# Kernel optimization log

Hardware: AMD Instinct MI355X
Metric: run time of the kernel (lower is better)

Reference implementation:

```python
import jax, jax.numpy as jnp
import numpy as np

N, n, m, k = 100000, 32, 16, 32
MU = 100.0  # bubble kernel scale (init arg mu)


def setup_inputs() -> dict:
    key = jax.random.key(0)
    ks = jax.random.split(key, 7)
    x = jax.random.normal(ks[0], (N,), dtype=jnp.float32)
    # torch.nn.Linear(N, n): weight [n, N], bias [n]
    encoder_w = jax.random.normal(ks[1], (n, N), dtype=jnp.float32) / np.float32(np.sqrt(N))
    encoder_b = jnp.zeros((n,), dtype=jnp.float32)
    # decoder parameter [n, N]
    decoder = jax.random.normal(ks[2], (n, N), dtype=jnp.float32) / np.float32(np.sqrt(n))
    # torch.nn.Linear(n, n*m): weight [n*m, n], bias [n*m]
    bw_w = jax.random.normal(ks[3], (n * m, n), dtype=jnp.float32) / np.float32(np.sqrt(n))
    bw_b = jnp.zeros((n * m,), dtype=jnp.float32)
    neighbour_distance = jax.random.uniform(ks[4], (N, k), dtype=jnp.float32)
    neighbour_id = jax.random.randint(ks[5], (N, k), 0, N)
    clustering_labels = jax.random.randint(ks[6], (N,), 0, m)
    return {
        "x": x,
        "encoder_w": encoder_w,
        "encoder_b": encoder_b,
        "decoder": decoder,
        "bw_w": bw_w,
        "bw_b": bw_b,
        "neighbour_distance": neighbour_distance,
        "neighbour_id": neighbour_id,
        "clustering_labels": clustering_labels,
    }


def reference(x, encoder_w, encoder_b, decoder, bw_w, bw_b,
              neighbour_distance, neighbour_id, clustering_labels):
    # encode: [N] -> [n]
    encoded = x @ encoder_w.T + encoder_b
    # per-basis, per-cluster bandwidths: sigmoid(Linear)/60 -> [n, m] -> expand to [n, N]
    bandwidths = jax.nn.sigmoid(encoded @ bw_w.T + bw_b) / 60.0
    w = bandwidths.reshape(n, m)[:, clustering_labels]  # [n, N]
    # bubble window: relu(1 - d^2 / (w*mu)^2) -> [n, N, k]
    window = jax.nn.relu(1.0 - neighbour_distance[None, :, :] ** 2
                         / (w[:, :, None] * MU) ** 2)
    # normalization over axis 1 (the N axis), faithful to the source's dim=1
    window = window / jnp.sum(window, axis=1, keepdims=True)
    # gather decoder rows at neighbours, weight, reduce over k: [n, N]
    convolved_basis = jnp.sum(decoder[:, neighbour_id] * window, axis=-1)
    # [n] @ [n, N] -> [N]
    return encoded @ convolved_basis
```

## Files before the change

### kernel.cpp

```cpp
#include <hip/hip_runtime.h>
#include <hip/hip_fp16.h>

#define N_PTS 100000
#define MU_F  100.0f

typedef unsigned int uint;
typedef _Float16 h2 __attribute__((ext_vector_type(2)));

#define E_SCALE 16384.0f
#define E_SCALE_INV (1.0f / 16384.0f)

#define ENC_BLKS 256
#define TR_BLKS  1563
#define HIST_BLKS 64

__global__ __launch_bounds__(256) void k_prep(const float* __restrict__ x,
                                              const float* __restrict__ encW,
                                              const float* __restrict__ encB,
                                              const float* __restrict__ dec,
                                              const int* __restrict__ labels,
                                              float* __restrict__ enc,
                                              __half* __restrict__ decT,
                                              int* __restrict__ ghist) {
    int b = blockIdx.x;
    if (b < ENC_BLKS) {
        int row = b & 31;
        int chunk = b >> 5;
        const int CH = N_PTS / 8;
        int base = chunk * CH;
        const float4* W4 = reinterpret_cast<const float4*>(encW + (size_t)row * N_PTS + base);
        const float4* x4 = reinterpret_cast<const float4*>(x + base);
        const int nv = CH / 4;
        float acc = 0.f;
        for (int idx = threadIdx.x; idx < nv; idx += 256) {
            float4 w = W4[idx];
            float4 xv = x4[idx];
            acc += w.x * xv.x + w.y * xv.y + w.z * xv.z + w.w * xv.w;
        }
        #pragma unroll
        for (int off = 32; off > 0; off >>= 1) acc += __shfl_down(acc, off);
        __shared__ float sred[4];
        int wid = threadIdx.x >> 6;
        if ((threadIdx.x & 63) == 0) sred[wid] = acc;
        __syncthreads();
        if (threadIdx.x == 0) {
            float s = sred[0] + sred[1] + sred[2] + sred[3];
            if (chunk == 0) s += encB[row];
            atomicAdd(enc + row, s);
        }
    } else if (b < ENC_BLKS + TR_BLKS) {
        __shared__ float tile[32][65];
        int j0 = (b - ENC_BLKS) * 64;
        int col = threadIdx.x & 63;
        int r0 = threadIdx.x >> 6;
        #pragma unroll
        for (int it = 0; it < 8; ++it) {
            int row = it * 4 + r0;
            int j = j0 + col;
            float v = (j < N_PTS) ? dec[(size_t)row * N_PTS + j] : 0.f;
            tile[row][col] = v;
        }
        __syncthreads();
        #pragma unroll
        for (int it = 0; it < 4; ++it) {
            int idx = it * 256 + threadIdx.x;
            int j = idx >> 4;
            int p = idx & 15;
            int jj = j0 + j;
            if (jj < N_PTS) {
                __half2 h = __halves2half2(__float2half(tile[2 * p][j]),
                                           __float2half(tile[2 * p + 1][j]));
                *reinterpret_cast<__half2*>(decT + (size_t)jj * 32 + 2 * p) = h;
            }
        }
    } else {
        __shared__ int lh[16];
        if (threadIdx.x < 16) lh[threadIdx.x] = 0;
        __syncthreads();
        int hb = b - (ENC_BLKS + TR_BLKS);
        for (int j = hb * 256 + threadIdx.x; j < N_PTS; j += HIST_BLKS * 256)
            atomicAdd(&lh[labels[j]], 1);
        __syncthreads();
        if (threadIdx.x < 16) atomicAdd(&ghist[threadIdx.x], lh[threadIdx.x]);
    }
}

__global__ __launch_bounds__(256) void k_scatter(const int* __restrict__ labels,
                                                 const int* __restrict__ ghist,
                                                 int* __restrict__ gcursor,
                                                 int* __restrict__ perm) {
    __shared__ int lh[16], lbase[16], lcur[16], gb[16];
    const int CHUNK = 784;
    int start = blockIdx.x * CHUNK;
    int end = min(start + CHUNK, N_PTS);
    if (threadIdx.x < 16) { lh[threadIdx.x] = 0; lcur[threadIdx.x] = 0; }
    if (threadIdx.x == 0) {
        int run = 0;
        for (int c = 0; c < 16; ++c) { gb[c] = run; run += ghist[c]; }
    }
    __syncthreads();
    for (int j = start + threadIdx.x; j < end; j += 256)
        atomicAdd(&lh[labels[j]], 1);
    __syncthreads();
    if (threadIdx.x < 16)
        lbase[threadIdx.x] = gb[threadIdx.x] + atomicAdd(&gcursor[threadIdx.x], lh[threadIdx.x]);
    __syncthreads();
    for (int j = start + threadIdx.x; j < end; j += 256) {
        int c = labels[j];
        int lpos = atomicAdd(&lcur[c], 1);
        perm[lbase[c] + lpos] = j;
    }
}

__device__ inline void build_invC(const float* __restrict__ encL,
                                  const float* __restrict__ bw_w,
                                  const float* __restrict__ bw_b,
                                  float* __restrict__ invCL, int c) {
    if (threadIdx.x < 32) {
        int r = threadIdx.x * 16 + c;
        float z = bw_b[r];
        const float* wr = bw_w + r * 32;
        #pragma unroll
        for (int p = 0; p < 32; ++p) z = fmaf(encL[p], wr[p], z);
        float s = 1.f / (1.f + __expf(-z));
        float wmu = s * (MU_F / 60.0f);
        invCL[threadIdx.x] = 1.f / (wmu * wmu);
    }
}

__global__ __launch_bounds__(512, 4) void k_S_sorted(const float* __restrict__ enc_g,
                                                     const float* __restrict__ bw_w,
                                                     const float* __restrict__ bw_b,
                                                     const float* __restrict__ nd,
                                                     const int* __restrict__ perm,
                                                     const int* __restrict__ ghist,
                                                     float* __restrict__ S,
                                                     float* __restrict__ S_part) {
    __shared__ float encL[32], invCL[32];
    __shared__ float Sloc[512];
    __shared__ int baseSh[17];
    int b = blockIdx.x;
    int c = b & 15;
    int ih = (b >> 4) & 1;
    int ch = b >> 5;
    if (threadIdx.x < 32) encL[threadIdx.x] = enc_g[threadIdx.x];
    if (threadIdx.x < 512) Sloc[threadIdx.x] = 0.f;
    if (threadIdx.x == 0) {
        int run = 0;
        for (int cc = 0; cc < 16; ++cc) { baseSh[cc] = run; run += ghist[cc]; }
        baseSh[16] = run;
    }
    __syncthreads();
    build_invC(encL, bw_w, bw_b, invCL, c);
    __syncthreads();

    float invC[16];
    #pragma unroll
    for (int i = 0; i < 16; ++i) invC[i] = invCL[ih * 16 + i];

    int bs = baseSh[c];
    int cnt = baseSh[c + 1] - bs;
    int lane = threadIdx.x & 63;
    int kk = lane & 31;
    int jh = lane >> 5;
    int gw = ch * 8 + (threadIdx.x >> 6);
    const int nw = 16 * 8;
    int npairs = (cnt + 1) >> 1;

    float acc[16];
    #pragma unroll
    for (int i = 0; i < 16; ++i) acc[i] = 0.f;

    for (int pp = gw; pp < npairs; pp += nw) {
        bool valid = (2 * pp + jh) < cnt;
        int p = valid ? (bs + 2 * pp + jh) : bs;
        int j = __builtin_nontemporal_load(&perm[p]);
        float d = __builtin_nontemporal_load(&nd[(size_t)j * 32 + kk]);
        float d2 = valid ? d * d : 1e30f;
        #pragma unroll
        for (int i = 0; i < 16; ++i)
            acc[i] += fmaxf(fmaf(-d2, invC[i], 1.0f), 0.f);
    }
    #pragma unroll
    for (int i = 0; i < 16; ++i) acc[i] += __shfl_xor(acc[i], 32);
    if (jh == 0) {
        #pragma unroll
        for (int i = 0; i < 16; ++i) atomicAdd(&Sloc[i * 32 + kk], acc[i]);
    }
    __syncthreads();
    if (S_part) {
        if (threadIdx.x < 512)
            S_part[(size_t)b * 512 + threadIdx.x] = Sloc[threadIdx.x];
    } else {
        if (threadIdx.x < 512) {
            float v = Sloc[threadIdx.x];
            if (v != 0.f)
                atomicAdd(&S[(ih * 16 + (threadIdx.x >> 5)) * 32 + (threadIdx.x & 31)], v);
        }
    }
}

__global__ __launch_bounds__(256) void k_S_reduce(const float* __restrict__ S_part,
                                                  float* __restrict__ S) {
    int g = blockIdx.x >> 2;
    int t = (blockIdx.x & 3) * 256 + threadIdx.x;
    int ih = t >> 9;
    int p = t & 511;
    float s = 0.f;
    #pragma unroll
    for (int c = 0; c < 16; ++c) {
        int b = c + (ih << 4) + (g << 5);
        s += S_part[(size_t)b * 512 + p];
    }
    atomicAdd(&S[t], s);
}

__global__ __launch_bounds__(256, 6) void k_main(const float* __restrict__ enc_g,
                                                 const float* __restrict__ bw_w,
                                                 const float* __restrict__ bw_b,
                                                 const float* __restrict__ S_g,
                                                 const float* __restrict__ nd,
                                                 const int* __restrict__ nid,
                                                 const int* __restrict__ perm,
                                                 const int* __restrict__ ghist,
                                                 const __half* __restrict__ decT,
                                                 float* __restrict__ out) {
    __shared__ float encL[32], invCL[32];
    __shared__ float ELf[1024];
    __shared__ int baseSh[17];
    int c = blockIdx.x & 15;
    int ch = blockIdx.x >> 4;
    if (threadIdx.x < 32) encL[threadIdx.x] = enc_g[threadIdx.x];
    if (threadIdx.x == 0) {
        int run = 0;
        for (int cc = 0; cc < 16; ++cc) { baseSh[cc] = run; run += ghist[cc]; }
        baseSh[16] = run;
    }
    __syncthreads();
    build_invC(encL, bw_w, bw_b, invCL, c);
    for (int t = threadIdx.x; t < 1024; t += 256)
        ELf[t] = encL[t >> 5] / S_g[t] * E_SCALE;
    __syncthreads();

    int lane = threadIdx.x & 63;
    int kk = lane & 31;
    int jh = lane >> 5;
    int R = lane >> 2;
    int q = lane & 3;

    float invq[8];
    h2 EhA[4], EhB[4];
    #pragma unroll
    for (int t = 0; t < 8; ++t) invq[t] = invCL[q * 8 + t];
    #pragma unroll
    for (int t = 0; t < 4; ++t) {
        int i0 = q * 8 + 2 * t, i1 = i0 + 1;
        EhA[t] = __builtin_bit_cast(h2, __builtin_amdgcn_cvt_pkrtz(
                     ELf[i0 * 32 + R], ELf[i1 * 32 + R]));
        EhB[t] = __builtin_bit_cast(h2, __builtin_amdgcn_cvt_pkrtz(
                     ELf[i0 * 32 + R + 16], ELf[i1 * 32 + R + 16]));
    }

    int bs = baseSh[c];
    int cnt = baseSh[c + 1] - bs;
    int wv = ch * 4 + (threadIdx.x >> 6);
    const int nw = 96 * 4;
    int npairs = (cnt + 1) >> 1;
    const uint4* decQ = reinterpret_cast<const uint4*>(decT);

    int pp = wv;
    int jl = 0, idl = 0; float d2l = 1e30f; bool validl = false;
    if (pp < npairs) {
        validl = (2 * pp + jh) < cnt;
        int p = validl ? (bs + 2 * pp + jh) : bs;
        jl = __builtin_nontemporal_load(&perm[p]);
        float d = __builtin_nontemporal_load(&nd[(size_t)jl * 32 + kk]);
        idl = __builtin_nontemporal_load(&nid[(size_t)jl * 32 + kk]);
        d2l = validl ? d * d : 1e30f;
    }

    while (pp < npairs) {
        int pn = pp + nw;
        int   id0 = __shfl(idl, 0 * 16 + R);
        int   id1 = __shfl(idl, 1 * 16 + R);
        int   id2 = __shfl(idl, 2 * 16 + R);
        int   id3 = __shfl(idl, 3 * 16 + R);
        float d20 = __shfl(d2l, 0 * 16 + R);
        float d21 = __shfl(d2l, 1 * 16 + R);
        float d22 = __shfl(d2l, 2 * 16 + R);
        float d23 = __shfl(d2l, 3 * 16 + R);
        uint4 r0 = decQ[(size_t)id0 * 4 + q];
        uint4 r1 = decQ[(size_t)id1 * 4 + q];
        uint4 r2 = decQ[(size_t)id2 * 4 + q];
        uint4 r3 = decQ[(size_t)id3 * 4 + q];
        int jn = 0, idn = 0; float d2n = 1e30f; bool validn = false;
        if (pn < npairs) {
            validn = (2 * pn + jh) < cnt;
            int p = validn ? (bs + 2 * pn + jh) : bs;
            jn = __builtin_nontemporal_load(&perm[p]);
            float d = __builtin_nontemporal_load(&nd[(size_t)jn * 32 + kk]);
            idn = __builtin_nontemporal_load(&nid[(size_t)jn * 32 + kk]);
            d2n = validn ? d * d : 1e30f;
        }

        float a0 = 0.f, a1 = 0.f, a2 = 0.f, a3 = 0.f;
        #pragma unroll
        for (int t = 0; t < 4; ++t) {
            uint dw0 = (t == 0) ? r0.x : (t == 1) ? r0.y : (t == 2) ? r0.z : r0.w;
            uint dw1 = (t == 0) ? r1.x : (t == 1) ? r1.y : (t == 2) ? r1.z : r1.w;
            uint dw2 = (t == 0) ? r2.x : (t == 1) ? r2.y : (t == 2) ? r2.z : r2.w;
            uint dw3 = (t == 0) ? r3.x : (t == 1) ? r3.y : (t == 2) ? r3.z : r3.w;
            float i0v = invq[2 * t], i1v = invq[2 * t + 1];
            {
                float w0 = fmaxf(fmaf(-d20, i0v, 1.f), 0.f);
                float w1 = fmaxf(fmaf(-d20, i1v, 1.f), 0.f);
                h2 wh = __builtin_bit_cast(h2, __builtin_amdgcn_cvt_pkrtz(w0, w1));
                a0 = __builtin_amdgcn_fdot2(wh * EhA[t], __builtin_bit_cast(h2, dw0), a0, false);
            }
            {
                float w0 = fmaxf(fmaf(-d21, i0v, 1.f), 0.f);
                float w1 = fmaxf(fmaf(-d21, i1v, 1.f), 0.f);
                h2 wh = __builtin_bit_cast(h2, __builtin_amdgcn_cvt_pkrtz(w0, w1));
                a1 = __builtin_amdgcn_fdot2(wh * EhB[t], __builtin_bit_cast(h2, dw1), a1, false);
            }
            {
                float w0 = fmaxf(fmaf(-d22, i0v, 1.f), 0.f);
                float w1 = fmaxf(fmaf(-d22, i1v, 1.f), 0.f);
                h2 wh = __builtin_bit_cast(h2, __builtin_amdgcn_cvt_pkrtz(w0, w1));
                a2 = __builtin_amdgcn_fdot2(wh * EhA[t], __builtin_bit_cast(h2, dw2), a2, false);
            }
            {
                float w0 = fmaxf(fmaf(-d23, i0v, 1.f), 0.f);
                float w1 = fmaxf(fmaf(-d23, i1v, 1.f), 0.f);
                h2 wh = __builtin_bit_cast(h2, __builtin_amdgcn_cvt_pkrtz(w0, w1));
                a3 = __builtin_amdgcn_fdot2(wh * EhB[t], __builtin_bit_cast(h2, dw3), a3, false);
            }
        }
        float u = a0 + a1;
        float v = a2 + a3;
        #pragma unroll
        for (int off = 32; off > 0; off >>= 1) {
            u += __shfl_xor(u, off);
            v += __shfl_xor(v, off);
        }
        if (lane == 0) out[jl] = u * E_SCALE_INV;
        if (lane == 32 && validl) out[jl] = v * E_SCALE_INV;

        jl = jn; idl = idn; d2l = d2n; validl = validn;
        pp = pn;
    }
}

extern "C" void kernel_launch(void* const* d_in, const int* in_sizes, int n_in,
                              void* d_out, int out_size, void* d_ws, size_t ws_size,
                              hipStream_t stream) {
    const float* x     = (const float*)d_in[0];
    const float* enc_w = (const float*)d_in[1];
    const float* enc_b = (const float*)d_in[2];
    const float* dec   = (const float*)d_in[3];
    const float* bw_w  = (const float*)d_in[4];
    const float* bw_b  = (const float*)d_in[5];
    const float* nd    = (const float*)d_in[6];
    const int*   nid   = (const int*)d_in[7];
    const int*   labels= (const int*)d_in[8];
    float* out = (float*)d_out;

    char* ws = (char*)d_ws;
    float* enc    = (float*)(ws + 0);
    float* S      = (float*)(ws + 128);
    int* ghist    = (int*)(ws + 4224);
    int* gcursor  = (int*)(ws + 4288);
    int* perm     = (int*)(ws + 8192);
    __half* decT  = (__half*)(ws + 408576);
    bool use_part = ws_size >= 7860224ull;
    float* S_part = use_part ? (float*)(ws + 6811648) : nullptr;

    (void)hipMemsetAsync(d_ws, 0, 4352, stream);
    k_prep<<<dim3(ENC_BLKS + TR_BLKS + HIST_BLKS), dim3(256), 0, stream>>>(
        x, enc_w, enc_b, dec, labels, enc, decT, ghist);
    k_scatter<<<dim3(128), dim3(256), 0, stream>>>(labels, ghist, gcursor, perm);
    k_S_sorted<<<dim3(512), dim3(512), 0, stream>>>(enc, bw_w, bw_b, nd, perm,
                                                    ghist, S, S_part);
    if (use_part)
        k_S_reduce<<<dim3(64), dim3(256), 0, stream>>>(S_part, S);
    k_main<<<dim3(1536), dim3(256), 0, stream>>>(enc, bw_w, bw_b, S, nd, nid,
                                                 perm, ghist, decT, out);
}
```

Measured before the change: 183.2 us.

## Deepen k_main prefetch pipeline and restructure S kernel to cover all 32 bases

k_S_sorted now has each 256-thread block accumulate all 32 basis rows instead of half, doubling the block count and the per-block partial buffer. k_S_reduce is rewritten to match the new partial layout. k_main drops the shuffle-based broadcast of neighbour ids and distances: each lane now loads its own ids and distances directly. It also adds a two-stage-ahead software prefetch of perm indices and id/distance rows to hide gather latency. The cost is more registers (32 accumulators, extra prefetch state) and a larger workspace requirement for the partial-sum path.

```diff
diff --git a/kernel.cpp b/kernel.cpp
--- a/kernel.cpp
+++ b/kernel.cpp
@@ -128,7 +128,7 @@
     }
 }
 
-__global__ __launch_bounds__(512, 4) void k_S_sorted(const float* __restrict__ enc_g,
+__global__ __launch_bounds__(256, 4) void k_S_sorted(const float* __restrict__ enc_g,
                                                      const float* __restrict__ bw_w,
                                                      const float* __restrict__ bw_b,
                                                      const float* __restrict__ nd,
@@ -137,14 +137,13 @@
                                                      float* __restrict__ S,
                                                      float* __restrict__ S_part) {
     __shared__ float encL[32], invCL[32];
-    __shared__ float Sloc[512];
+    __shared__ float Sloc[1024];
     __shared__ int baseSh[17];
     int b = blockIdx.x;
     int c = b & 15;
-    int ih = (b >> 4) & 1;
-    int ch = b >> 5;
+    int ch = b >> 4;
     if (threadIdx.x < 32) encL[threadIdx.x] = enc_g[threadIdx.x];
-    if (threadIdx.x < 512) Sloc[threadIdx.x] = 0.f;
+    for (int t = threadIdx.x; t < 1024; t += 256) Sloc[t] = 0.f;
     if (threadIdx.x == 0) {
         int run = 0;
         for (int cc = 0; cc < 16; ++cc) { baseSh[cc] = run; run += ghist[cc]; }
@@ -154,22 +153,22 @@
     build_invC(encL, bw_w, bw_b, invCL, c);
     __syncthreads();
 
-    float invC[16];
-    #pragma unroll
-    for (int i = 0; i < 16; ++i) invC[i] = invCL[ih * 16 + i];
+    float invC[32];
+    #pragma unroll
+    for (int i = 0; i < 32; ++i) invC[i] = invCL[i];
 
     int bs = baseSh[c];
     int cnt = baseSh[c + 1] - bs;
     int lane = threadIdx.x & 63;
     int kk = lane & 31;
     int jh = lane >> 5;
-    int gw = ch * 8 + (threadIdx.x >> 6);
-    const int nw = 16 * 8;
+    int gw = ch * 4 + (threadIdx.x >> 6);
+    const int nw = 64 * 4;
     int npairs = (cnt + 1) >> 1;
 
-    float acc[16];
-    #pragma unroll
-    for (int i = 0; i < 16; ++i) acc[i] = 0.f;
+    float acc[32];
+    #pragma unroll
+    for (int i = 0; i < 32; ++i) acc[i] = 0.f;
 
     for (int pp = gw; pp < npairs; pp += nw) {
         bool valid = (2 * pp + jh) < cnt;
@@ -178,40 +177,35 @@
         float d = __builtin_nontemporal_load(&nd[(size_t)j * 32 + kk]);
         float d2 = valid ? d * d : 1e30f;
         #pragma unroll
-        for (int i = 0; i < 16; ++i)
+        for (int i = 0; i < 32; ++i)
             acc[i] += fmaxf(fmaf(-d2, invC[i], 1.0f), 0.f);
     }
     #pragma unroll
-    for (int i = 0; i < 16; ++i) acc[i] += __shfl_xor(acc[i], 32);
+    for (int i = 0; i < 32; ++i) acc[i] += __shfl_xor(acc[i], 32);
     if (jh == 0) {
         #pragma unroll
-        for (int i = 0; i < 16; ++i) atomicAdd(&Sloc[i * 32 + kk], acc[i]);
+        for (int i = 0; i < 32; ++i) atomicAdd(&Sloc[i * 32 + kk], acc[i]);
     }
     __syncthreads();
     if (S_part) {
-        if (threadIdx.x < 512)
-            S_part[(size_t)b * 512 + threadIdx.x] = Sloc[threadIdx.x];
+        for (int t = threadIdx.x; t < 1024; t += 256)
+            S_part[(size_t)b * 1024 + t] = Sloc[t];
     } else {
-        if (threadIdx.x < 512) {
-            float v = Sloc[threadIdx.x];
-            if (v != 0.f)
-                atomicAdd(&S[(ih * 16 + (threadIdx.x >> 5)) * 32 + (threadIdx.x & 31)], v);
-        }
-    }
-}
-
-__global__ __launch_bounds__(256) void k_S_reduce(const float* __restrict__ S_part,
-                                                  float* __restrict__ S) {
-    int g = blockIdx.x >> 2;
-    int t = (blockIdx.x & 3) * 256 + threadIdx.x;
-    int ih = t >> 9;
-    int p = t & 511;
+        for (int t = threadIdx.x; t < 1024; t += 256) {
+            float v = Sloc[t];
+            if (v != 0.f) atomicAdd(&S[t], v);
+        }
+    }
+}
+
+__global__ __launch_bounds__(1024) void k_S_reduce(const float* __restrict__ S_part,
+                                                   float* __restrict__ S) {
+    int g = blockIdx.x;
+    int t = threadIdx.x;
     float s = 0.f;
     #pragma unroll
-    for (int c = 0; c < 16; ++c) {
-        int b = c + (ih << 4) + (g << 5);
-        s += S_part[(size_t)b * 512 + p];
-    }
+    for (int u = 0; u < 16; ++u)
+        s += S_part[(size_t)(g * 16 + u) * 1024 + t];
     atomicAdd(&S[t], s);
 }
 
@@ -243,8 +237,6 @@
     __syncthreads();
 
     int lane = threadIdx.x & 63;
-    int kk = lane & 31;
-    int jh = lane >> 5;
     int R = lane >> 2;
     int q = lane & 3;
 
@@ -268,40 +260,46 @@
     int npairs = (cnt + 1) >> 1;
     const uint4* decQ = reinterpret_cast<const uint4*>(decT);
 
+    if (wv >= npairs) return;
+
+    auto load_pair = [&](int pp, int& j0, int& j1, bool& v1) {
+        bool ok = pp < npairs;
+        int p0 = ok ? (bs + 2 * pp) : bs;
+        v1 = ok && ((2 * pp + 1) < cnt);
+        j0 = perm[p0];
+        j1 = perm[v1 ? p0 + 1 : p0];
+    };
+    auto load_ids = [&](int j0, int j1, int* id, float* dd) {
+        #pragma unroll
+        for (int s = 0; s < 4; ++s) {
+            int jj = (s >> 1) ? j1 : j0;
+            size_t idx = (size_t)jj * 32 + (s & 1) * 16 + R;
+            id[s] = __builtin_nontemporal_load(&nid[idx]);
+            dd[s] = __builtin_nontemporal_load(&nd[idx]);
+        }
+    };
+
     int pp = wv;
-    int jl = 0, idl = 0; float d2l = 1e30f; bool validl = false;
-    if (pp < npairs) {
-        validl = (2 * pp + jh) < cnt;
-        int p = validl ? (bs + 2 * pp + jh) : bs;
-        jl = __builtin_nontemporal_load(&perm[p]);
-        float d = __builtin_nontemporal_load(&nd[(size_t)jl * 32 + kk]);
-        idl = __builtin_nontemporal_load(&nid[(size_t)jl * 32 + kk]);
-        d2l = validl ? d * d : 1e30f;
-    }
+    int j0a, j1a, j0b, j1b; bool v1a, v1b;
+    int ida[4]; float dda[4];
+    load_pair(pp, j0a, j1a, v1a);
+    load_ids(j0a, j1a, ida, dda);
+    load_pair(pp + nw, j0b, j1b, v1b);
 
     while (pp < npairs) {
-        int pn = pp + nw;
-        int   id0 = __shfl(idl, 0 * 16 + R);
-        int   id1 = __shfl(idl, 1 * 16 + R);
-        int   id2 = __shfl(idl, 2 * 16 + R);
-        int   id3 = __shfl(idl, 3 * 16 + R);
-        float d20 = __shfl(d2l, 0 * 16 + R);
-        float d21 = __shfl(d2l, 1 * 16 + R);
-        float d22 = __shfl(d2l, 2 * 16 + R);
-        float d23 = __shfl(d2l, 3 * 16 + R);
-        uint4 r0 = decQ[(size_t)id0 * 4 + q];
-        uint4 r1 = decQ[(size_t)id1 * 4 + q];
-        uint4 r2 = decQ[(size_t)id2 * 4 + q];
-        uint4 r3 = decQ[(size_t)id3 * 4 + q];
-        int jn = 0, idn = 0; float d2n = 1e30f; bool validn = false;
-        if (pn < npairs) {
-            validn = (2 * pn + jh) < cnt;
-            int p = validn ? (bs + 2 * pn + jh) : bs;
-            jn = __builtin_nontemporal_load(&perm[p]);
-            float d = __builtin_nontemporal_load(&nd[(size_t)jn * 32 + kk]);
-            idn = __builtin_nontemporal_load(&nid[(size_t)jn * 32 + kk]);
-            d2n = validn ? d * d : 1e30f;
-        }
+        uint4 r0 = decQ[(size_t)ida[0] * 4 + q];
+        uint4 r1 = decQ[(size_t)ida[1] * 4 + q];
+        uint4 r2 = decQ[(size_t)ida[2] * 4 + q];
+        uint4 r3 = decQ[(size_t)ida[3] * 4 + q];
+        int idb[4]; float ddb[4];
+        load_ids(j0b, j1b, idb, ddb);
+        int j0c, j1c; bool v1c;
+        load_pair(pp + 2 * nw, j0c, j1c, v1c);
+
+        float d20 = dda[0] * dda[0];
+        float d21 = dda[1] * dda[1];
+        float d22 = dda[2] * dda[2];
+        float d23 = dda[3] * dda[3];
 
         float a0 = 0.f, a1 = 0.f, a2 = 0.f, a3 = 0.f;
         #pragma unroll
@@ -343,11 +341,14 @@
             u += __shfl_xor(u, off);
             v += __shfl_xor(v, off);
         }
-        if (lane == 0) out[jl] = u * E_SCALE_INV;
-        if (lane == 32 && validl) out[jl] = v * E_SCALE_INV;
-
-        jl = jn; idl = idn; d2l = d2n; validl = validn;
-        pp = pn;
+        if (lane == 0) out[j0a] = u * E_SCALE_INV;
+        if (lane == 32 && v1a) out[j1a] = v * E_SCALE_INV;
+
+        j0a = j0b; j1a = j1b; v1a = v1b;
+        j0b = j0c; j1b = j1c; v1b = v1c;
+        #pragma unroll
+        for (int s = 0; s < 4; ++s) { ida[s] = idb[s]; dda[s] = ddb[s]; }
+        pp += nw;
     }
 }
 
@@ -372,17 +373,17 @@
     int* gcursor  = (int*)(ws + 4288);
     int* perm     = (int*)(ws + 8192);
     __half* decT  = (__half*)(ws + 408576);
-    bool use_part = ws_size >= 7860224ull;
+    bool use_part = ws_size >= 11005952ull;
     float* S_part = use_part ? (float*)(ws + 6811648) : nullptr;
 
     (void)hipMemsetAsync(d_ws, 0, 4352, stream);
     k_prep<<<dim3(ENC_BLKS + TR_BLKS + HIST_BLKS), dim3(256), 0, stream>>>(
         x, enc_w, enc_b, dec, labels, enc, decT, ghist);
     k_scatter<<<dim3(128), dim3(256), 0, stream>>>(labels, ghist, gcursor, perm);
-    k_S_sorted<<<dim3(512), dim3(512), 0, stream>>>(enc, bw_w, bw_b, nd, perm,
-                                                    ghist, S, S_part);
+    k_S_sorted<<<dim3(1024), dim3(256), 0, stream>>>(enc, bw_w, bw_b, nd, perm,
+                                                     ghist, S, S_part);
     if (use_part)
-        k_S_reduce<<<dim3(64), dim3(256), 0, stream>>>(S_part, S);
+        k_S_reduce<<<dim3(64), dim3(1024), 0, stream>>>(S_part, S);
     k_main<<<dim3(1536), dim3(256), 0, stream>>>(enc, bw_w, bw_b, S, nd, nid,
                                                  perm, ghist, decT, out);
 }
```

New measurement: 187.3 us. 1.02x slower.
